# Kernel optimization log

Hardware: AMD Instinct MI355X
Metric: run time of the kernel (lower is better)

Reference implementation:

```python
import jax, jax.numpy as jnp
import numpy as np

B, N, HID, HEADS = 4, 512, 64, 4
D = HID // HEADS          # head_dim = 16
E_DIM = 1
SCALE = 1.0 / np.sqrt(D)
LN_EPS = 1e-5
NEG = -1e9


def _linear_init(k, fan_in, fan_out):
    lim = 1.0 / np.sqrt(fan_in)
    kw, kb = jax.random.split(k)
    W = jax.random.uniform(kw, (fan_in, fan_out), jnp.float32, -lim, lim)
    b = jax.random.uniform(kb, (fan_out,), jnp.float32, -lim, lim)
    return W, b


def setup_inputs() -> dict:
    key = jax.random.key(0)
    ks = jax.random.split(key, 8)
    W1_w, W1_b = _linear_init(ks[3], HID, HID)
    W2_w, W2_b = _linear_init(ks[4], HID, HID)
    W3_w, W3_b = _linear_init(ks[5], HID, HID)
    W4_w, W4_b = _linear_init(ks[6], HID, HID)
    W5_w, W5_b = _linear_init(ks[7], E_DIM, HID)
    return {
        "x": jax.random.normal(ks[0], (B, N, HID), jnp.float32),
        "adj": jax.random.randint(ks[1], (B, N, N), 0, 2, jnp.int32),
        "edge_features": jax.random.normal(ks[2], (B, N, N, E_DIM), jnp.float32),
        "W1_w": W1_w, "W1_b": W1_b,
        "W2_w": W2_w, "W2_b": W2_b,
        "W3_w": W3_w, "W3_b": W3_b,
        "W4_w": W4_w, "W4_b": W4_b,
        "W5_w": W5_w, "W5_b": W5_b,
        "ln_g": jnp.ones((HID,), jnp.float32),
        "ln_b": jnp.zeros((HID,), jnp.float32),
    }


def _layer_norm(y, g, b):
    m = jnp.mean(y, axis=-1, keepdims=True)
    v = jnp.mean(jnp.square(y - m), axis=-1, keepdims=True)
    return (y - m) * jax.lax.rsqrt(v + LN_EPS) * g + b


def reference(x, adj, edge_features, W1_w, W1_b, W2_w, W2_b, W3_w, W3_b,
              W4_w, W4_b, W5_w, W5_b, ln_g, ln_b):
    b, n, h = x.shape
    self_t = x @ W1_w + W1_b                               # [B,N,HID]
    Q = (x @ W3_w + W3_b).reshape(b, n, HEADS, D)          # [B,N,H,D]
    K = (x @ W4_w + W4_b).reshape(b, n, HEADS, D)          # [B,N,H,D]
    # edge contribution: W5 e_ij -> [B,N,N,H,D] (the big intermediate)
    Ec = (edge_features @ W5_w + W5_b).reshape(b, n, n, HEADS, D)
    # (Q_i . (K_j + E_ij)) split into node-pair GEMM + edge broadcast term
    scores = (jnp.einsum('bihd,bjhd->bhij', Q, K)
              + jnp.einsum('bihd,bijhd->bhij', Q, Ec)) * SCALE  # [B,H,N,N]
    scores = jnp.where(adj[:, None, :, :] == 0, NEG, scores)
    attn = jax.nn.softmax(scores, axis=-1)                 # dropout = identity (eval)
    V = (x @ W2_w + W2_b).reshape(b, n, HEADS, D)          # [B,N,H,D]
    msg = jnp.einsum('bhij,bjhd->bihd', attn, V).reshape(b, n, h)
    return _layer_norm(x + self_t + msg, ln_g, ln_b)
```

## Files before the change

### kernel.cpp

```cpp
#include <hip/hip_runtime.h>

#define B 4
#define N 512
#define HID 64
#define HEADS 4
#define DH 16
#define SCALE 0.25f
#define NEG (-1e9f)
#define LN_EPS 1e-5f

constexpr int ROWS = B * N;
constexpr size_t OFF_ST  = 0;
constexpr size_t OFF_Q   = (size_t)ROWS * HID;
constexpr size_t OFF_K   = 2 * OFF_Q;
constexpr size_t OFF_V   = 3 * OFF_Q;
constexpr size_t OFF_MSG = 4 * OFF_Q;

__global__ __launch_bounds__(256) void proj_kernel(
    const float* __restrict__ x,
    const float* __restrict__ W1w, const float* __restrict__ W1b,
    const float* __restrict__ W2w, const float* __restrict__ W2b,
    const float* __restrict__ W3w, const float* __restrict__ W3b,
    const float* __restrict__ W4w, const float* __restrict__ W4b,
    float* __restrict__ ws)
{
  __shared__ float xsT[64 * 20];
  const int t = threadIdx.x;
  const int rows0 = blockIdx.x * 16;

  {
    const float4 v = *(const float4*)&x[(size_t)rows0 * HID + t * 4];
    const int r = t >> 4;
    const int k0 = (t & 15) * 4;
    xsT[(k0 + 0) * 20 + r] = v.x;
    xsT[(k0 + 1) * 20 + r] = v.y;
    xsT[(k0 + 2) * 20 + r] = v.z;
    xsT[(k0 + 3) * 20 + r] = v.w;
  }
  __syncthreads();

  const int m = t >> 6;
  const int c = t & 63;
  const float* Ww; const float* Wb; size_t off;
  if      (m == 0) { Ww = W1w; Wb = W1b; off = OFF_ST; }
  else if (m == 1) { Ww = W3w; Wb = W3b; off = OFF_Q;  }
  else if (m == 2) { Ww = W4w; Wb = W4b; off = OFF_K;  }
  else             { Ww = W2w; Wb = W2b; off = OFF_V;  }

  float acc[16];
#pragma unroll
  for (int r = 0; r < 16; ++r) acc[r] = 0.f;

#pragma unroll 8
  for (int k = 0; k < 64; ++k) {
    const float w = Ww[(k << 6) + c];
    const float* xr = &xsT[k * 20];
    const float4 a0 = *(const float4*)(xr);
    const float4 a1 = *(const float4*)(xr + 4);
    const float4 a2 = *(const float4*)(xr + 8);
    const float4 a3 = *(const float4*)(xr + 12);
    acc[0]  = fmaf(a0.x, w, acc[0]);  acc[1]  = fmaf(a0.y, w, acc[1]);
    acc[2]  = fmaf(a0.z, w, acc[2]);  acc[3]  = fmaf(a0.w, w, acc[3]);
    acc[4]  = fmaf(a1.x, w, acc[4]);  acc[5]  = fmaf(a1.y, w, acc[5]);
    acc[6]  = fmaf(a1.z, w, acc[6]);  acc[7]  = fmaf(a1.w, w, acc[7]);
    acc[8]  = fmaf(a2.x, w, acc[8]);  acc[9]  = fmaf(a2.y, w, acc[9]);
    acc[10] = fmaf(a2.z, w, acc[10]); acc[11] = fmaf(a2.w, w, acc[11]);
    acc[12] = fmaf(a3.x, w, acc[12]); acc[13] = fmaf(a3.y, w, acc[13]);
    acc[14] = fmaf(a3.z, w, acc[14]); acc[15] = fmaf(a3.w, w, acc[15]);
  }

  const float bias = Wb[c];
  const size_t base = off + (size_t)rows0 * HID + c;
#pragma unroll
  for (int r = 0; r < 16; ++r)
    ws[base + (size_t)r * HID] = acc[r] + bias;
}

__global__ __launch_bounds__(256, 2) void attn_kernel(
    const int*   __restrict__ adj,
    const float* __restrict__ efeat,
    const float* __restrict__ W5w, const float* __restrict__ W5b,
    float* __restrict__ ws)
{
  __shared__ float Ksh[N * 20];
  __shared__ float Vsh[N * 20];

  const int it = blockIdx.x, h = blockIdx.y, b = blockIdx.z;
  const int t = threadIdx.x;
  const int g  = t & 15;
  const int il = t >> 4;
  const int i  = it * 16 + il;

  const float* Qb = ws + OFF_Q;
  const float* Kb = ws + OFF_K;
  const float* Vb = ws + OFF_V;
  float* msg = ws + OFF_MSG;

  {
    const int jj = t >> 2;
    const int dq = (t & 3) << 2;
#pragma unroll
    for (int p = 0; p < 8; ++p) {
      const int j = jj + (p << 6);
      const size_t gb = ((size_t)(b * N + j)) * HID + h * DH + dq;
      *(float4*)&Ksh[j * 20 + dq] = *(const float4*)&Kb[gb];
      *(float4*)&Vsh[j * 20 + dq] = *(const float4*)&Vb[gb];
    }
  }

  const float* qrow = Qb + ((size_t)(b * N + i)) * HID + h * DH;
  const float4 q0 = *(const float4*)(qrow);
  const float4 q1 = *(const float4*)(qrow + 4);
  const float4 q2 = *(const float4*)(qrow + 8);
  const float4 q3 = *(const float4*)(qrow + 12);
  const float4 w50 = *(const float4*)&W5w[h * DH];
  const float4 w51 = *(const float4*)&W5w[h * DH + 4];
  const float4 w52 = *(const float4*)&W5w[h * DH + 8];
  const float4 w53 = *(const float4*)&W5w[h * DH + 12];
  const float4 b50 = *(const float4*)&W5b[h * DH];
  const float4 b51 = *(const float4*)&W5b[h * DH + 4];
  const float4 b52 = *(const float4*)&W5b[h * DH + 8];
  const float4 b53 = *(const float4*)&W5b[h * DH + 12];
  float qw5 = q0.x*w50.x + q0.y*w50.y + q0.z*w50.z + q0.w*w50.w
            + q1.x*w51.x + q1.y*w51.y + q1.z*w51.z + q1.w*w51.w
            + q2.x*w52.x + q2.y*w52.y + q2.z*w52.z + q2.w*w52.w
            + q3.x*w53.x + q3.y*w53.y + q3.z*w53.z + q3.w*w53.w;
  float qb5 = q0.x*b50.x + q0.y*b50.y + q0.z*b50.z + q0.w*b50.w
            + q1.x*b51.x + q1.y*b51.y + q1.z*b51.z + q1.w*b51.w
            + q2.x*b52.x + q2.y*b52.y + q2.z*b52.z + q2.w*b52.w
            + q3.x*b53.x + q3.y*b53.y + q3.z*b53.z + q3.w*b53.w;

  __syncthreads();

  const int*   adjRow = adj   + ((size_t)(b * N + i)) * N;
  const float* eRow   = efeat + ((size_t)(b * N + i)) * N;

  float m = -3.0e38f, l = 0.f;
  float acc[16];
#pragma unroll
  for (int d = 0; d < 16; ++d) acc[d] = 0.f;

  for (int jj = 0; jj < 32; ++jj) {
    const int j = g + (jj << 4);
    const int   a  = adjRow[j];
    const float ev = eRow[j];
    const float* kr = &Ksh[j * 20];
    const float4 k0 = *(const float4*)(kr);
    const float4 k1 = *(const float4*)(kr + 4);
    const float4 k2 = *(const float4*)(kr + 8);
    const float4 k3 = *(const float4*)(kr + 12);
    float sA = q0.x*k0.x, sB = q0.y*k0.y, sC = q0.z*k0.z, sD = q0.w*k0.w;
    sA = fmaf(q1.x, k1.x, sA); sB = fmaf(q1.y, k1.y, sB);
    sC = fmaf(q1.z, k1.z, sC); sD = fmaf(q1.w, k1.w, sD);
    sA = fmaf(q2.x, k2.x, sA); sB = fmaf(q2.y, k2.y, sB);
    sC = fmaf(q2.z, k2.z, sC); sD = fmaf(q2.w, k2.w, sD);
    sA = fmaf(q3.x, k3.x, sA); sB = fmaf(q3.y, k3.y, sB);
    sC = fmaf(q3.z, k3.z, sC); sD = fmaf(q3.w, k3.w, sD);
    float s = ((sA + sB) + (sC + sD) + ev * qw5 + qb5) * SCALE;
    s = (a == 0) ? NEG : s;

    float p;
    if (s > m) {
      const float sc = __expf(m - s);
      l *= sc;
#pragma unroll
      for (int d = 0; d < 16; ++d) acc[d] *= sc;
      m = s;
      p = 1.f;
    } else {
      p = __expf(s - m);
    }
    l += p;

    const float* vr = &Vsh[j * 20];
    const float4 v0 = *(const float4*)(vr);
    const float4 v1 = *(const float4*)(vr + 4);
    const float4 v2 = *(const float4*)(vr + 8);
    const float4 v3 = *(const float4*)(vr + 12);
    acc[0]  = fmaf(p, v0.x, acc[0]);  acc[1]  = fmaf(p, v0.y, acc[1]);
    acc[2]  = fmaf(p, v0.z, acc[2]);  acc[3]  = fmaf(p, v0.w, acc[3]);
    acc[4]  = fmaf(p, v1.x, acc[4]);  acc[5]  = fmaf(p, v1.y, acc[5]);
    acc[6]  = fmaf(p, v1.z, acc[6]);  acc[7]  = fmaf(p, v1.w, acc[7]);
    acc[8]  = fmaf(p, v2.x, acc[8]);  acc[9]  = fmaf(p, v2.y, acc[9]);
    acc[10] = fmaf(p, v2.z, acc[10]); acc[11] = fmaf(p, v2.w, acc[11]);
    acc[12] = fmaf(p, v3.x, acc[12]); acc[13] = fmaf(p, v3.y, acc[13]);
    acc[14] = fmaf(p, v3.z, acc[14]); acc[15] = fmaf(p, v3.w, acc[15]);
  }

  float M = m;
#pragma unroll
  for (int o = 1; o < 16; o <<= 1) M = fmaxf(M, __shfl_xor(M, o, 16));
  const float wgt = __expf(m - M);
  float lw = l * wgt;
#pragma unroll
  for (int o = 1; o < 16; o <<= 1) lw += __shfl_xor(lw, o, 16);

  __syncthreads();
  float* P = Ksh;
  const int prow = (il * 16 + g) * 20;
  *(float4*)&P[prow +  0] = make_float4(acc[0]*wgt,  acc[1]*wgt,  acc[2]*wgt,  acc[3]*wgt);
  *(float4*)&P[prow +  4] = make_float4(acc[4]*wgt,  acc[5]*wgt,  acc[6]*wgt,  acc[7]*wgt);
  *(float4*)&P[prow +  8] = make_float4(acc[8]*wgt,  acc[9]*wgt,  acc[10]*wgt, acc[11]*wgt);
  *(float4*)&P[prow + 12] = make_float4(acc[12]*wgt, acc[13]*wgt, acc[14]*wgt, acc[15]*wgt);
  __syncthreads();

  float ssum = 0.f;
#pragma unroll
  for (int gp = 0; gp < 16; ++gp)
    ssum += P[(il * 16 + gp) * 20 + g];

  msg[((size_t)(b * N + i)) * HID + h * DH + g] = ssum * (1.0f / lw);
}

__global__ __launch_bounds__(256) void ln_kernel(
    const float* __restrict__ x, const float* __restrict__ ws,
    const float* __restrict__ gamma, const float* __restrict__ beta,
    float* __restrict__ out)
{
  const int t = threadIdx.x;
  const int lane = t & 63;
  const int row = blockIdx.x * 4 + (t >> 6);
  const size_t idx = (size_t)row * HID + lane;
  const float* ST  = ws + OFF_ST;
  const float* MSG = ws + OFF_MSG;

  const float v = x[idx] + ST[idx] + MSG[idx];
  float mu = v;
#pragma unroll
  for (int o = 1; o < 64; o <<= 1) mu += __shfl_xor(mu, o, 64);
  mu *= (1.0f / 64.0f);
  const float dv = v - mu;
  float var = dv * dv;
#pragma unroll
  for (int o = 1; o < 64; o <<= 1) var += __shfl_xor(var, o, 64);
  var *= (1.0f / 64.0f);
  out[idx] = dv * rsqrtf(var + LN_EPS) * gamma[lane] + beta[lane];
}

extern "C" void kernel_launch(void* const* d_in, const int* in_sizes, int n_in,
                              void* d_out, int out_size, void* d_ws, size_t ws_size,
                              hipStream_t stream)
{
  const float* x   = (const float*)d_in[0];
  const int*   adj = (const int*)d_in[1];
  const float* ef  = (const float*)d_in[2];
  const float* W1w = (const float*)d_in[3];
  const float* W1b = (const float*)d_in[4];
  const float* W2w = (const float*)d_in[5];
  const float* W2b = (const float*)d_in[6];
  const float* W3w = (const float*)d_in[7];
  const float* W3b = (const float*)d_in[8];
  const float* W4w = (const float*)d_in[9];
  const float* W4b = (const float*)d_in[10];
  const float* W5w = (const float*)d_in[11];
  const float* W5b = (const float*)d_in[12];
  const float* lng = (const float*)d_in[13];
  const float* lnb = (const float*)d_in[14];
  float* ws  = (float*)d_ws;
  float* out = (float*)d_out;

  proj_kernel<<<128, 256, 0, stream>>>(x, W1w, W1b, W2w, W2b, W3w, W3b, W4w, W4b, ws);
  attn_kernel<<<dim3(32, HEADS, B), 256, 0, stream>>>(adj, ef, W5w, W5b, ws);
  ln_kernel<<<ROWS / 4, 256, 0, stream>>>(x, ws, lng, lnb, out);
}
```

Measured before the change: 27.04 us.

## Process two query rows per thread in attention and shrink projection row tiles

The attention kernel now computes two query rows per thread, so each block covers 32 rows and reuses the K/V tiles it stages in shared memory. This halves the grid and the total K/V staging traffic. The adjacency and edge-feature loads for the next column are prefetched one iteration ahead to hide global latency. The projection kernel drops to 8 rows per block, which doubles the block count to spread work across more CUs. The risk is lower occupancy in the attention kernel (about one block per CU) and more register pressure from the doubled accumulators.

```diff
diff --git a/kernel.cpp b/kernel.cpp
--- a/kernel.cpp
+++ b/kernel.cpp
@@ -24,18 +24,18 @@
     const float* __restrict__ W4w, const float* __restrict__ W4b,
     float* __restrict__ ws)
 {
-  __shared__ float xsT[64 * 20];
+  __shared__ float xsT[64 * 8];
   const int t = threadIdx.x;
-  const int rows0 = blockIdx.x * 16;
-
-  {
+  const int rows0 = blockIdx.x * 8;
+
+  if (t < 128) {
     const float4 v = *(const float4*)&x[(size_t)rows0 * HID + t * 4];
     const int r = t >> 4;
     const int k0 = (t & 15) * 4;
-    xsT[(k0 + 0) * 20 + r] = v.x;
-    xsT[(k0 + 1) * 20 + r] = v.y;
-    xsT[(k0 + 2) * 20 + r] = v.z;
-    xsT[(k0 + 3) * 20 + r] = v.w;
+    xsT[(k0 + 0) * 8 + r] = v.x;
+    xsT[(k0 + 1) * 8 + r] = v.y;
+    xsT[(k0 + 2) * 8 + r] = v.z;
+    xsT[(k0 + 3) * 8 + r] = v.w;
   }
   __syncthreads();
 
@@ -47,32 +47,26 @@
   else if (m == 2) { Ww = W4w; Wb = W4b; off = OFF_K;  }
   else             { Ww = W2w; Wb = W2b; off = OFF_V;  }
 
-  float acc[16];
-#pragma unroll
-  for (int r = 0; r < 16; ++r) acc[r] = 0.f;
-
-#pragma unroll 8
+  float acc[8];
+#pragma unroll
+  for (int r = 0; r < 8; ++r) acc[r] = 0.f;
+
+#pragma unroll 16
   for (int k = 0; k < 64; ++k) {
     const float w = Ww[(k << 6) + c];
-    const float* xr = &xsT[k * 20];
+    const float* xr = &xsT[k * 8];
     const float4 a0 = *(const float4*)(xr);
     const float4 a1 = *(const float4*)(xr + 4);
-    const float4 a2 = *(const float4*)(xr + 8);
-    const float4 a3 = *(const float4*)(xr + 12);
-    acc[0]  = fmaf(a0.x, w, acc[0]);  acc[1]  = fmaf(a0.y, w, acc[1]);
-    acc[2]  = fmaf(a0.z, w, acc[2]);  acc[3]  = fmaf(a0.w, w, acc[3]);
-    acc[4]  = fmaf(a1.x, w, acc[4]);  acc[5]  = fmaf(a1.y, w, acc[5]);
-    acc[6]  = fmaf(a1.z, w, acc[6]);  acc[7]  = fmaf(a1.w, w, acc[7]);
-    acc[8]  = fmaf(a2.x, w, acc[8]);  acc[9]  = fmaf(a2.y, w, acc[9]);
-    acc[10] = fmaf(a2.z, w, acc[10]); acc[11] = fmaf(a2.w, w, acc[11]);
-    acc[12] = fmaf(a3.x, w, acc[12]); acc[13] = fmaf(a3.y, w, acc[13]);
-    acc[14] = fmaf(a3.z, w, acc[14]); acc[15] = fmaf(a3.w, w, acc[15]);
+    acc[0] = fmaf(a0.x, w, acc[0]); acc[1] = fmaf(a0.y, w, acc[1]);
+    acc[2] = fmaf(a0.z, w, acc[2]); acc[3] = fmaf(a0.w, w, acc[3]);
+    acc[4] = fmaf(a1.x, w, acc[4]); acc[5] = fmaf(a1.y, w, acc[5]);
+    acc[6] = fmaf(a1.z, w, acc[6]); acc[7] = fmaf(a1.w, w, acc[7]);
   }
 
   const float bias = Wb[c];
   const size_t base = off + (size_t)rows0 * HID + c;
 #pragma unroll
-  for (int r = 0; r < 16; ++r)
+  for (int r = 0; r < 8; ++r)
     ws[base + (size_t)r * HID] = acc[r] + bias;
 }
 
@@ -89,7 +83,9 @@
   const int t = threadIdx.x;
   const int g  = t & 15;
   const int il = t >> 4;
-  const int i  = it * 16 + il;
+  const int i0 = it * 32;
+  const int iA = i0 + il;
+  const int iB = iA + 16;
 
   const float* Qb = ws + OFF_Q;
   const float* Kb = ws + OFF_K;
@@ -108,11 +104,6 @@
     }
   }
 
-  const float* qrow = Qb + ((size_t)(b * N + i)) * HID + h * DH;
-  const float4 q0 = *(const float4*)(qrow);
-  const float4 q1 = *(const float4*)(qrow + 4);
-  const float4 q2 = *(const float4*)(qrow + 8);
-  const float4 q3 = *(const float4*)(qrow + 12);
   const float4 w50 = *(const float4*)&W5w[h * DH];
   const float4 w51 = *(const float4*)&W5w[h * DH + 4];
   const float4 w52 = *(const float4*)&W5w[h * DH + 8];
@@ -121,95 +112,157 @@
   const float4 b51 = *(const float4*)&W5b[h * DH + 4];
   const float4 b52 = *(const float4*)&W5b[h * DH + 8];
   const float4 b53 = *(const float4*)&W5b[h * DH + 12];
-  float qw5 = q0.x*w50.x + q0.y*w50.y + q0.z*w50.z + q0.w*w50.w
-            + q1.x*w51.x + q1.y*w51.y + q1.z*w51.z + q1.w*w51.w
-            + q2.x*w52.x + q2.y*w52.y + q2.z*w52.z + q2.w*w52.w
-            + q3.x*w53.x + q3.y*w53.y + q3.z*w53.z + q3.w*w53.w;
-  float qb5 = q0.x*b50.x + q0.y*b50.y + q0.z*b50.z + q0.w*b50.w
-            + q1.x*b51.x + q1.y*b51.y + q1.z*b51.z + q1.w*b51.w
-            + q2.x*b52.x + q2.y*b52.y + q2.z*b52.z + q2.w*b52.w
-            + q3.x*b53.x + q3.y*b53.y + q3.z*b53.z + q3.w*b53.w;
+
+  float4 qA0, qA1, qA2, qA3, qB0, qB1, qB2, qB3;
+  float qw5A, qb5A, qw5B, qb5B;
+  {
+    const float* qr = Qb + ((size_t)(b * N + iA)) * HID + h * DH;
+    qA0 = *(const float4*)(qr);     qA1 = *(const float4*)(qr + 4);
+    qA2 = *(const float4*)(qr + 8); qA3 = *(const float4*)(qr + 12);
+    qw5A = qA0.x*w50.x + qA0.y*w50.y + qA0.z*w50.z + qA0.w*w50.w
+         + qA1.x*w51.x + qA1.y*w51.y + qA1.z*w51.z + qA1.w*w51.w
+         + qA2.x*w52.x + qA2.y*w52.y + qA2.z*w52.z + qA2.w*w52.w
+         + qA3.x*w53.x + qA3.y*w53.y + qA3.z*w53.z + qA3.w*w53.w;
+    qb5A = qA0.x*b50.x + qA0.y*b50.y + qA0.z*b50.z + qA0.w*b50.w
+         + qA1.x*b51.x + qA1.y*b51.y + qA1.z*b51.z + qA1.w*b51.w
+         + qA2.x*b52.x + qA2.y*b52.y + qA2.z*b52.z + qA2.w*b52.w
+         + qA3.x*b53.x + qA3.y*b53.y + qA3.z*b53.z + qA3.w*b53.w;
+  }
+  {
+    const float* qr = Qb + ((size_t)(b * N + iB)) * HID + h * DH;
+    qB0 = *(const float4*)(qr);     qB1 = *(const float4*)(qr + 4);
+    qB2 = *(const float4*)(qr + 8); qB3 = *(const float4*)(qr + 12);
+    qw5B = qB0.x*w50.x + qB0.y*w50.y + qB0.z*w50.z + qB0.w*w50.w
+         + qB1.x*w51.x + qB1.y*w51.y + qB1.z*w51.z + qB1.w*w51.w
+         + qB2.x*w52.x + qB2.y*w52.y + qB2.z*w52.z + qB2.w*w52.w
+         + qB3.x*w53.x + qB3.y*w53.y + qB3.z*w53.z + qB3.w*w53.w;
+    qb5B = qB0.x*b50.x + qB0.y*b50.y + qB0.z*b50.z + qB0.w*b50.w
+         + qB1.x*b51.x + qB1.y*b51.y + qB1.z*b51.z + qB1.w*b51.w
+         + qB2.x*b52.x + qB2.y*b52.y + qB2.z*b52.z + qB2.w*b52.w
+         + qB3.x*b53.x + qB3.y*b53.y + qB3.z*b53.z + qB3.w*b53.w;
+  }
 
   __syncthreads();
 
-  const int*   adjRow = adj   + ((size_t)(b * N + i)) * N;
-  const float* eRow   = efeat + ((size_t)(b * N + i)) * N;
-
-  float m = -3.0e38f, l = 0.f;
-  float acc[16];
-#pragma unroll
-  for (int d = 0; d < 16; ++d) acc[d] = 0.f;
+  const int*   adjA = adj   + ((size_t)(b * N + iA)) * N;
+  const int*   adjB = adj   + ((size_t)(b * N + iB)) * N;
+  const float* eA   = efeat + ((size_t)(b * N + iA)) * N;
+  const float* eB   = efeat + ((size_t)(b * N + iB)) * N;
+
+  float mA = -3.0e38f, lA = 0.f, mB = -3.0e38f, lB = 0.f;
+  float accA[16], accB[16];
+#pragma unroll
+  for (int d = 0; d < 16; ++d) { accA[d] = 0.f; accB[d] = 0.f; }
+
+  int   aAv = adjA[g], aBv = adjB[g];
+  float eAv = eA[g],   eBv = eB[g];
 
   for (int jj = 0; jj < 32; ++jj) {
     const int j = g + (jj << 4);
-    const int   a  = adjRow[j];
-    const float ev = eRow[j];
+    const int jn = (j + 16) & (N - 1);
+    const int   naA = adjA[jn], naB = adjB[jn];
+    const float neA = eA[jn],   neB = eB[jn];
+
     const float* kr = &Ksh[j * 20];
     const float4 k0 = *(const float4*)(kr);
     const float4 k1 = *(const float4*)(kr + 4);
     const float4 k2 = *(const float4*)(kr + 8);
     const float4 k3 = *(const float4*)(kr + 12);
-    float sA = q0.x*k0.x, sB = q0.y*k0.y, sC = q0.z*k0.z, sD = q0.w*k0.w;
-    sA = fmaf(q1.x, k1.x, sA); sB = fmaf(q1.y, k1.y, sB);
-    sC = fmaf(q1.z, k1.z, sC); sD = fmaf(q1.w, k1.w, sD);
-    sA = fmaf(q2.x, k2.x, sA); sB = fmaf(q2.y, k2.y, sB);
-    sC = fmaf(q2.z, k2.z, sC); sD = fmaf(q2.w, k2.w, sD);
-    sA = fmaf(q3.x, k3.x, sA); sB = fmaf(q3.y, k3.y, sB);
-    sC = fmaf(q3.z, k3.z, sC); sD = fmaf(q3.w, k3.w, sD);
-    float s = ((sA + sB) + (sC + sD) + ev * qw5 + qb5) * SCALE;
-    s = (a == 0) ? NEG : s;
-
-    float p;
-    if (s > m) {
-      const float sc = __expf(m - s);
-      l *= sc;
-#pragma unroll
-      for (int d = 0; d < 16; ++d) acc[d] *= sc;
-      m = s;
-      p = 1.f;
-    } else {
-      p = __expf(s - m);
-    }
-    l += p;
+
+    float sA = qA0.x*k0.x + qA0.y*k0.y + qA0.z*k0.z + qA0.w*k0.w;
+    sA = fmaf(qA1.x,k1.x, fmaf(qA1.y,k1.y, fmaf(qA1.z,k1.z, fmaf(qA1.w,k1.w, sA))));
+    sA = fmaf(qA2.x,k2.x, fmaf(qA2.y,k2.y, fmaf(qA2.z,k2.z, fmaf(qA2.w,k2.w, sA))));
+    sA = fmaf(qA3.x,k3.x, fmaf(qA3.y,k3.y, fmaf(qA3.z,k3.z, fmaf(qA3.w,k3.w, sA))));
+    float sB = qB0.x*k0.x + qB0.y*k0.y + qB0.z*k0.z + qB0.w*k0.w;
+    sB = fmaf(qB1.x,k1.x, fmaf(qB1.y,k1.y, fmaf(qB1.z,k1.z, fmaf(qB1.w,k1.w, sB))));
+    sB = fmaf(qB2.x,k2.x, fmaf(qB2.y,k2.y, fmaf(qB2.z,k2.z, fmaf(qB2.w,k2.w, sB))));
+    sB = fmaf(qB3.x,k3.x, fmaf(qB3.y,k3.y, fmaf(qB3.z,k3.z, fmaf(qB3.w,k3.w, sB))));
+
+    float s0 = (sA + eAv * qw5A + qb5A) * SCALE;
+    float s1 = (sB + eBv * qw5B + qb5B) * SCALE;
+    s0 = (aAv == 0) ? NEG : s0;
+    s1 = (aBv == 0) ? NEG : s1;
+
+    float pA, pB;
+    if (s0 > mA) {
+      const float sc = __expf(mA - s0);
+      lA *= sc;
+#pragma unroll
+      for (int d = 0; d < 16; ++d) accA[d] *= sc;
+      mA = s0; pA = 1.f;
+    } else pA = __expf(s0 - mA);
+    lA += pA;
+    if (s1 > mB) {
+      const float sc = __expf(mB - s1);
+      lB *= sc;
+#pragma unroll
+      for (int d = 0; d < 16; ++d) accB[d] *= sc;
+      mB = s1; pB = 1.f;
+    } else pB = __expf(s1 - mB);
+    lB += pB;
 
     const float* vr = &Vsh[j * 20];
     const float4 v0 = *(const float4*)(vr);
     const float4 v1 = *(const float4*)(vr + 4);
     const float4 v2 = *(const float4*)(vr + 8);
     const float4 v3 = *(const float4*)(vr + 12);
-    acc[0]  = fmaf(p, v0.x, acc[0]);  acc[1]  = fmaf(p, v0.y, acc[1]);
-    acc[2]  = fmaf(p, v0.z, acc[2]);  acc[3]  = fmaf(p, v0.w, acc[3]);
-    acc[4]  = fmaf(p, v1.x, acc[4]);  acc[5]  = fmaf(p, v1.y, acc[5]);
-    acc[6]  = fmaf(p, v1.z, acc[6]);  acc[7]  = fmaf(p, v1.w, acc[7]);
-    acc[8]  = fmaf(p, v2.x, acc[8]);  acc[9]  = fmaf(p, v2.y, acc[9]);
-    acc[10] = fmaf(p, v2.z, acc[10]); acc[11] = fmaf(p, v2.w, acc[11]);
-    acc[12] = fmaf(p, v3.x, acc[12]); acc[13] = fmaf(p, v3.y, acc[13]);
-    acc[14] = fmaf(p, v3.z, acc[14]); acc[15] = fmaf(p, v3.w, acc[15]);
-  }
-
-  float M = m;
-#pragma unroll
-  for (int o = 1; o < 16; o <<= 1) M = fmaxf(M, __shfl_xor(M, o, 16));
-  const float wgt = __expf(m - M);
-  float lw = l * wgt;
-#pragma unroll
-  for (int o = 1; o < 16; o <<= 1) lw += __shfl_xor(lw, o, 16);
+    accA[0] = fmaf(pA,v0.x,accA[0]); accA[1] = fmaf(pA,v0.y,accA[1]);
+    accA[2] = fmaf(pA,v0.z,accA[2]); accA[3] = fmaf(pA,v0.w,accA[3]);
+    accA[4] = fmaf(pA,v1.x,accA[4]); accA[5] = fmaf(pA,v1.y,accA[5]);
+    accA[6] = fmaf(pA,v1.z,accA[6]); accA[7] = fmaf(pA,v1.w,accA[7]);
+    accA[8] = fmaf(pA,v2.x,accA[8]); accA[9] = fmaf(pA,v2.y,accA[9]);
+    accA[10]= fmaf(pA,v2.z,accA[10]);accA[11]= fmaf(pA,v2.w,accA[11]);
+    accA[12]= fmaf(pA,v3.x,accA[12]);accA[13]= fmaf(pA,v3.y,accA[13]);
+    accA[14]= fmaf(pA,v3.z,accA[14]);accA[15]= fmaf(pA,v3.w,accA[15]);
+    accB[0] = fmaf(pB,v0.x,accB[0]); accB[1] = fmaf(pB,v0.y,accB[1]);
+    accB[2] = fmaf(pB,v0.z,accB[2]); accB[3] = fmaf(pB,v0.w,accB[3]);
+    accB[4] = fmaf(pB,v1.x,accB[4]); accB[5] = fmaf(pB,v1.y,accB[5]);
+    accB[6] = fmaf(pB,v1.z,accB[6]); accB[7] = fmaf(pB,v1.w,accB[7]);
+    accB[8] = fmaf(pB,v2.x,accB[8]); accB[9] = fmaf(pB,v2.y,accB[9]);
+    accB[10]= fmaf(pB,v2.z,accB[10]);accB[11]= fmaf(pB,v2.w,accB[11]);
+    accB[12]= fmaf(pB,v3.x,accB[12]);accB[13]= fmaf(pB,v3.y,accB[13]);
+    accB[14]= fmaf(pB,v3.z,accB[14]);accB[15]= fmaf(pB,v3.w,accB[15]);
+
+    aAv = naA; aBv = naB; eAv = neA; eBv = neB;
+  }
+
+  float MA = mA, MB = mB;
+#pragma unroll
+  for (int o = 1; o < 16; o <<= 1) {
+    MA = fmaxf(MA, __shfl_xor(MA, o, 16));
+    MB = fmaxf(MB, __shfl_xor(MB, o, 16));
+  }
+  const float wA = __expf(mA - MA);
+  const float wB = __expf(mB - MB);
+  float lwA = lA * wA, lwB = lB * wB;
+#pragma unroll
+  for (int o = 1; o < 16; o <<= 1) {
+    lwA += __shfl_xor(lwA, o, 16);
+    lwB += __shfl_xor(lwB, o, 16);
+  }
 
   __syncthreads();
   float* P = Ksh;
-  const int prow = (il * 16 + g) * 20;
-  *(float4*)&P[prow +  0] = make_float4(acc[0]*wgt,  acc[1]*wgt,  acc[2]*wgt,  acc[3]*wgt);
-  *(float4*)&P[prow +  4] = make_float4(acc[4]*wgt,  acc[5]*wgt,  acc[6]*wgt,  acc[7]*wgt);
-  *(float4*)&P[prow +  8] = make_float4(acc[8]*wgt,  acc[9]*wgt,  acc[10]*wgt, acc[11]*wgt);
-  *(float4*)&P[prow + 12] = make_float4(acc[12]*wgt, acc[13]*wgt, acc[14]*wgt, acc[15]*wgt);
+  const int baseA = (il * 16 + g) * 20;
+  const int baseB = ((il + 16) * 16 + g) * 20;
+  *(float4*)&P[baseA+ 0] = make_float4(accA[0]*wA, accA[1]*wA, accA[2]*wA, accA[3]*wA);
+  *(float4*)&P[baseA+ 4] = make_float4(accA[4]*wA, accA[5]*wA, accA[6]*wA, accA[7]*wA);
+  *(float4*)&P[baseA+ 8] = make_float4(accA[8]*wA, accA[9]*wA, accA[10]*wA,accA[11]*wA);
+  *(float4*)&P[baseA+12] = make_float4(accA[12]*wA,accA[13]*wA,accA[14]*wA,accA[15]*wA);
+  *(float4*)&P[baseB+ 0] = make_float4(accB[0]*wB, accB[1]*wB, accB[2]*wB, accB[3]*wB);
+  *(float4*)&P[baseB+ 4] = make_float4(accB[4]*wB, accB[5]*wB, accB[6]*wB, accB[7]*wB);
+  *(float4*)&P[baseB+ 8] = make_float4(accB[8]*wB, accB[9]*wB, accB[10]*wB,accB[11]*wB);
+  *(float4*)&P[baseB+12] = make_float4(accB[12]*wB,accB[13]*wB,accB[14]*wB,accB[15]*wB);
   __syncthreads();
 
-  float ssum = 0.f;
-#pragma unroll
-  for (int gp = 0; gp < 16; ++gp)
-    ssum += P[(il * 16 + gp) * 20 + g];
-
-  msg[((size_t)(b * N + i)) * HID + h * DH + g] = ssum * (1.0f / lw);
+  float sA2 = 0.f, sB2 = 0.f;
+#pragma unroll
+  for (int gp = 0; gp < 16; ++gp) {
+    sA2 += P[(il * 16 + gp) * 20 + g];
+    sB2 += P[((il + 16) * 16 + gp) * 20 + g];
+  }
+  msg[((size_t)(b * N + iA)) * HID + h * DH + g] = sA2 * (1.0f / lwA);
+  msg[((size_t)(b * N + iB)) * HID + h * DH + g] = sB2 * (1.0f / lwB);
 }
 
 __global__ __launch_bounds__(256) void ln_kernel(
@@ -259,7 +312,7 @@
   float* ws  = (float*)d_ws;
   float* out = (float*)d_out;
 
-  proj_kernel<<<128, 256, 0, stream>>>(x, W1w, W1b, W2w, W2b, W3w, W3b, W4w, W4b, ws);
-  attn_kernel<<<dim3(32, HEADS, B), 256, 0, stream>>>(adj, ef, W5w, W5b, ws);
+  proj_kernel<<<ROWS / 8, 256, 0, stream>>>(x, W1w, W1b, W2w, W2b, W3w, W3b, W4w, W4b, ws);
+  attn_kernel<<<dim3(16, HEADS, B), 256, 0, stream>>>(adj, ef, W5w, W5b, ws);
   ln_kernel<<<ROWS / 4, 256, 0, stream>>>(x, ws, lng, lnb, out);
 }
```

Result: slower. 27.77 us (+2.7%).

## Replace online softmax with two-pass max-then-exp and halve projection row tile

Applied to the files above, without the earlier changes.

The attention kernel now computes all 32 scores per thread into registers, takes the row max first, then does one exp-and-accumulate pass. This removes the data-dependent branch and the per-step rescaling of 16 accumulators that the online softmax needed. The projection kernel handles 8 rows per block instead of 16, which doubles its grid to give more parallelism. In exchange, register pressure in the attention kernel goes up (32 scores plus 16 accumulators), and each loaded weight is reused across fewer rows.

```diff
diff --git a/kernel.cpp b/kernel.cpp
--- a/kernel.cpp
+++ b/kernel.cpp
@@ -24,18 +24,18 @@
     const float* __restrict__ W4w, const float* __restrict__ W4b,
     float* __restrict__ ws)
 {
-  __shared__ float xsT[64 * 20];
+  __shared__ float xsT[64 * 8];
   const int t = threadIdx.x;
-  const int rows0 = blockIdx.x * 16;
-
-  {
+  const int rows0 = blockIdx.x * 8;
+
+  if (t < 128) {
     const float4 v = *(const float4*)&x[(size_t)rows0 * HID + t * 4];
     const int r = t >> 4;
     const int k0 = (t & 15) * 4;
-    xsT[(k0 + 0) * 20 + r] = v.x;
-    xsT[(k0 + 1) * 20 + r] = v.y;
-    xsT[(k0 + 2) * 20 + r] = v.z;
-    xsT[(k0 + 3) * 20 + r] = v.w;
+    xsT[(k0 + 0) * 8 + r] = v.x;
+    xsT[(k0 + 1) * 8 + r] = v.y;
+    xsT[(k0 + 2) * 8 + r] = v.z;
+    xsT[(k0 + 3) * 8 + r] = v.w;
   }
   __syncthreads();
 
@@ -47,32 +47,26 @@
   else if (m == 2) { Ww = W4w; Wb = W4b; off = OFF_K;  }
   else             { Ww = W2w; Wb = W2b; off = OFF_V;  }
 
-  float acc[16];
-#pragma unroll
-  for (int r = 0; r < 16; ++r) acc[r] = 0.f;
-
-#pragma unroll 8
+  float acc[8];
+#pragma unroll
+  for (int r = 0; r < 8; ++r) acc[r] = 0.f;
+
+#pragma unroll 16
   for (int k = 0; k < 64; ++k) {
     const float w = Ww[(k << 6) + c];
-    const float* xr = &xsT[k * 20];
+    const float* xr = &xsT[k * 8];
     const float4 a0 = *(const float4*)(xr);
     const float4 a1 = *(const float4*)(xr + 4);
-    const float4 a2 = *(const float4*)(xr + 8);
-    const float4 a3 = *(const float4*)(xr + 12);
-    acc[0]  = fmaf(a0.x, w, acc[0]);  acc[1]  = fmaf(a0.y, w, acc[1]);
-    acc[2]  = fmaf(a0.z, w, acc[2]);  acc[3]  = fmaf(a0.w, w, acc[3]);
-    acc[4]  = fmaf(a1.x, w, acc[4]);  acc[5]  = fmaf(a1.y, w, acc[5]);
-    acc[6]  = fmaf(a1.z, w, acc[6]);  acc[7]  = fmaf(a1.w, w, acc[7]);
-    acc[8]  = fmaf(a2.x, w, acc[8]);  acc[9]  = fmaf(a2.y, w, acc[9]);
-    acc[10] = fmaf(a2.z, w, acc[10]); acc[11] = fmaf(a2.w, w, acc[11]);
-    acc[12] = fmaf(a3.x, w, acc[12]); acc[13] = fmaf(a3.y, w, acc[13]);
-    acc[14] = fmaf(a3.z, w, acc[14]); acc[15] = fmaf(a3.w, w, acc[15]);
+    acc[0] = fmaf(a0.x, w, acc[0]); acc[1] = fmaf(a0.y, w, acc[1]);
+    acc[2] = fmaf(a0.z, w, acc[2]); acc[3] = fmaf(a0.w, w, acc[3]);
+    acc[4] = fmaf(a1.x, w, acc[4]); acc[5] = fmaf(a1.y, w, acc[5]);
+    acc[6] = fmaf(a1.z, w, acc[6]); acc[7] = fmaf(a1.w, w, acc[7]);
   }
 
   const float bias = Wb[c];
   const size_t base = off + (size_t)rows0 * HID + c;
 #pragma unroll
-  for (int r = 0; r < 16; ++r)
+  for (int r = 0; r < 8; ++r)
     ws[base + (size_t)r * HID] = acc[r] + bias;
 }
 
@@ -121,25 +115,22 @@
   const float4 b51 = *(const float4*)&W5b[h * DH + 4];
   const float4 b52 = *(const float4*)&W5b[h * DH + 8];
   const float4 b53 = *(const float4*)&W5b[h * DH + 12];
-  float qw5 = q0.x*w50.x + q0.y*w50.y + q0.z*w50.z + q0.w*w50.w
-            + q1.x*w51.x + q1.y*w51.y + q1.z*w51.z + q1.w*w51.w
-            + q2.x*w52.x + q2.y*w52.y + q2.z*w52.z + q2.w*w52.w
-            + q3.x*w53.x + q3.y*w53.y + q3.z*w53.z + q3.w*w53.w;
-  float qb5 = q0.x*b50.x + q0.y*b50.y + q0.z*b50.z + q0.w*b50.w
-            + q1.x*b51.x + q1.y*b51.y + q1.z*b51.z + q1.w*b51.w
-            + q2.x*b52.x + q2.y*b52.y + q2.z*b52.z + q2.w*b52.w
-            + q3.x*b53.x + q3.y*b53.y + q3.z*b53.z + q3.w*b53.w;
+  const float qw5 = q0.x*w50.x + q0.y*w50.y + q0.z*w50.z + q0.w*w50.w
+                  + q1.x*w51.x + q1.y*w51.y + q1.z*w51.z + q1.w*w51.w
+                  + q2.x*w52.x + q2.y*w52.y + q2.z*w52.z + q2.w*w52.w
+                  + q3.x*w53.x + q3.y*w53.y + q3.z*w53.z + q3.w*w53.w;
+  const float qb5 = q0.x*b50.x + q0.y*b50.y + q0.z*b50.z + q0.w*b50.w
+                  + q1.x*b51.x + q1.y*b51.y + q1.z*b51.z + q1.w*b51.w
+                  + q2.x*b52.x + q2.y*b52.y + q2.z*b52.z + q2.w*b52.w
+                  + q3.x*b53.x + q3.y*b53.y + q3.z*b53.z + q3.w*b53.w;
 
   __syncthreads();
 
   const int*   adjRow = adj   + ((size_t)(b * N + i)) * N;
   const float* eRow   = efeat + ((size_t)(b * N + i)) * N;
 
-  float m = -3.0e38f, l = 0.f;
-  float acc[16];
-#pragma unroll
-  for (int d = 0; d < 16; ++d) acc[d] = 0.f;
-
+  float s[32];
+#pragma unroll
   for (int jj = 0; jj < 32; ++jj) {
     const int j = g + (jj << 4);
     const int   a  = adjRow[j];
@@ -150,28 +141,40 @@
     const float4 k2 = *(const float4*)(kr + 8);
     const float4 k3 = *(const float4*)(kr + 12);
     float sA = q0.x*k0.x, sB = q0.y*k0.y, sC = q0.z*k0.z, sD = q0.w*k0.w;
-    sA = fmaf(q1.x, k1.x, sA); sB = fmaf(q1.y, k1.y, sB);
-    sC = fmaf(q1.z, k1.z, sC); sD = fmaf(q1.w, k1.w, sD);
-    sA = fmaf(q2.x, k2.x, sA); sB = fmaf(q2.y, k2.y, sB);
-    sC = fmaf(q2.z, k2.z, sC); sD = fmaf(q2.w, k2.w, sD);
-    sA = fmaf(q3.x, k3.x, sA); sB = fmaf(q3.y, k3.y, sB);
-    sC = fmaf(q3.z, k3.z, sC); sD = fmaf(q3.w, k3.w, sD);
-    float s = ((sA + sB) + (sC + sD) + ev * qw5 + qb5) * SCALE;
-    s = (a == 0) ? NEG : s;
-
-    float p;
-    if (s > m) {
-      const float sc = __expf(m - s);
-      l *= sc;
-#pragma unroll
-      for (int d = 0; d < 16; ++d) acc[d] *= sc;
-      m = s;
-      p = 1.f;
-    } else {
-      p = __expf(s - m);
-    }
-    l += p;
-
+    sA = fmaf(q1.x,k1.x,sA); sB = fmaf(q1.y,k1.y,sB);
+    sC = fmaf(q1.z,k1.z,sC); sD = fmaf(q1.w,k1.w,sD);
+    sA = fmaf(q2.x,k2.x,sA); sB = fmaf(q2.y,k2.y,sB);
+    sC = fmaf(q2.z,k2.z,sC); sD = fmaf(q2.w,k2.w,sD);
+    sA = fmaf(q3.x,k3.x,sA); sB = fmaf(q3.y,k3.y,sB);
+    sC = fmaf(q3.z,k3.z,sC); sD = fmaf(q3.w,k3.w,sD);
+    const float sc = ((sA + sB) + (sC + sD) + ev * qw5 + qb5) * SCALE;
+    s[jj] = (a == 0) ? NEG : sc;
+  }
+
+  float r16[16], r8[8], r4[4];
+#pragma unroll
+  for (int k = 0; k < 16; ++k) r16[k] = fmaxf(s[k], s[k + 16]);
+#pragma unroll
+  for (int k = 0; k < 8;  ++k) r8[k]  = fmaxf(r16[k], r16[k + 8]);
+#pragma unroll
+  for (int k = 0; k < 4;  ++k) r4[k]  = fmaxf(r8[k], r8[k + 4]);
+  float M = fmaxf(fmaxf(r4[0], r4[1]), fmaxf(r4[2], r4[3]));
+#pragma unroll
+  for (int o = 1; o < 16; o <<= 1) M = fmaxf(M, __shfl_xor(M, o, 16));
+
+  float l0 = 0.f, l1 = 0.f, l2 = 0.f, l3 = 0.f;
+  float acc[16];
+#pragma unroll
+  for (int d = 0; d < 16; ++d) acc[d] = 0.f;
+
+#pragma unroll
+  for (int jj = 0; jj < 32; ++jj) {
+    const int j = g + (jj << 4);
+    const float p = __expf(s[jj] - M);
+    if      ((jj & 3) == 0) l0 += p;
+    else if ((jj & 3) == 1) l1 += p;
+    else if ((jj & 3) == 2) l2 += p;
+    else                    l3 += p;
     const float* vr = &Vsh[j * 20];
     const float4 v0 = *(const float4*)(vr);
     const float4 v1 = *(const float4*)(vr + 4);
@@ -187,21 +190,17 @@
     acc[14] = fmaf(p, v3.z, acc[14]); acc[15] = fmaf(p, v3.w, acc[15]);
   }
 
-  float M = m;
-#pragma unroll
-  for (int o = 1; o < 16; o <<= 1) M = fmaxf(M, __shfl_xor(M, o, 16));
-  const float wgt = __expf(m - M);
-  float lw = l * wgt;
+  float lw = (l0 + l1) + (l2 + l3);
 #pragma unroll
   for (int o = 1; o < 16; o <<= 1) lw += __shfl_xor(lw, o, 16);
 
   __syncthreads();
   float* P = Ksh;
   const int prow = (il * 16 + g) * 20;
-  *(float4*)&P[prow +  0] = make_float4(acc[0]*wgt,  acc[1]*wgt,  acc[2]*wgt,  acc[3]*wgt);
-  *(float4*)&P[prow +  4] = make_float4(acc[4]*wgt,  acc[5]*wgt,  acc[6]*wgt,  acc[7]*wgt);
-  *(float4*)&P[prow +  8] = make_float4(acc[8]*wgt,  acc[9]*wgt,  acc[10]*wgt, acc[11]*wgt);
-  *(float4*)&P[prow + 12] = make_float4(acc[12]*wgt, acc[13]*wgt, acc[14]*wgt, acc[15]*wgt);
+  *(float4*)&P[prow +  0] = make_float4(acc[0],  acc[1],  acc[2],  acc[3]);
+  *(float4*)&P[prow +  4] = make_float4(acc[4],  acc[5],  acc[6],  acc[7]);
+  *(float4*)&P[prow +  8] = make_float4(acc[8],  acc[9],  acc[10], acc[11]);
+  *(float4*)&P[prow + 12] = make_float4(acc[12], acc[13], acc[14], acc[15]);
   __syncthreads();
 
   float ssum = 0.f;
@@ -259,7 +258,7 @@
   float* ws  = (float*)d_ws;
   float* out = (float*)d_out;
 
-  proj_kernel<<<128, 256, 0, stream>>>(x, W1w, W1b, W2w, W2b, W3w, W3b, W4w, W4b, ws);
+  proj_kernel<<<ROWS / 8, 256, 0, stream>>>(x, W1w, W1b, W2w, W2b, W3w, W3b, W4w, W4b, ws);
   attn_kernel<<<dim3(32, HEADS, B), 256, 0, stream>>>(adj, ef, W5w, W5b, ws);
   ln_kernel<<<ROWS / 4, 256, 0, stream>>>(x, ws, lng, lnb, out);
 }
```

New measurement: 24.00 us. 1.13x faster.
